# Performance work log

Hardware: AMD Instinct MI355X
Metric: run time of the kernel (lower is better)

The kernel has to match this reference:

```python
import itertools
import jax, jax.numpy as jnp
import numpy as np

B, RES = 256, 16
DIM, KEY_DIM, NUM_HEADS, ATTN_RATIO = 448, 32, 8, 4
SEQ = RES * RES
EXP_KEY_DIM = ATTN_RATIO * KEY_DIM          # 128
TOTAL_KEY = KEY_DIM * NUM_HEADS             # 256
TOTAL_EXP = EXP_KEY_DIM * NUM_HEADS         # 1024
QKV_DIM = TOTAL_EXP + 2 * TOTAL_KEY         # 1536
SCALE = KEY_DIM ** -0.5


def _build_bias_idxs():
    # Replicates the itertools.product loop from build()
    points = list(itertools.product(range(RES), range(RES)))
    offsets = {}
    idxs = []
    for p1 in points:
        for p2 in points:
            off = (abs(p1[0] - p2[0]), abs(p1[1] - p2[1]))
            if off not in offsets:
                offsets[off] = len(offsets)
            idxs.append(offsets[off])
    return np.asarray(idxs, dtype=np.int32).reshape(SEQ, SEQ), len(offsets)


def setup_inputs() -> dict:
    key = jax.random.key(0)
    ks = jax.random.split(key, 6)
    bias_idxs_np, n_off = _build_bias_idxs()
    std = 0.02
    return {
        "hidden_states": jax.random.normal(ks[0], (B, SEQ, DIM), dtype=jnp.float32),
        "qkv_w": jax.random.normal(ks[1], (DIM, QKV_DIM), dtype=jnp.float32) * std,
        "qkv_b": jnp.zeros((QKV_DIM,), dtype=jnp.float32),
        "proj_w": jax.random.normal(ks[2], (TOTAL_EXP, DIM), dtype=jnp.float32) * std,
        "proj_b": jnp.zeros((DIM,), dtype=jnp.float32),
        "attention_biases": jax.random.normal(ks[3], (NUM_HEADS, n_off), dtype=jnp.float32) * std,
        "attention_bias_idxs": jnp.asarray(bias_idxs_np),
    }


def reference(hidden_states, qkv_w, qkv_b, proj_w, proj_b, attention_biases, attention_bias_idxs):
    b, s, _ = hidden_states.shape
    qkv = hidden_states @ qkv_w + qkv_b                       # [B,S,1536]
    qkv = qkv.reshape(b, s, NUM_HEADS, KEY_DIM * 2 + EXP_KEY_DIM)
    q, k, v = jnp.split(qkv, [KEY_DIM, 2 * KEY_DIM], axis=3)  # [B,S,H,dk],[B,S,H,dk],[B,S,H,dv]
    scores = jnp.einsum("bqhd,bkhd->bhqk", q, k) * SCALE      # [B,H,S,S]
    bias = attention_biases[:, attention_bias_idxs]           # [H,S,S] gather
    probs = jax.nn.softmax(scores + bias[None], axis=-1)
    ctx = jnp.einsum("bhqk,bkhd->bqhd", probs, v)             # [B,S,H,dv]
    ctx = ctx.reshape(b, s, TOTAL_EXP)
    return ctx @ proj_w + proj_b
```

## Files before the change

### kernel.cpp

```cpp
#include <hip/hip_runtime.h>
#include <hip/hip_bf16.h>
#include <stdint.h>


typedef __attribute__((ext_vector_type(4))) float f32x4;
typedef __attribute__((ext_vector_type(8))) short short8;
typedef __attribute__((ext_vector_type(4))) unsigned short u16x4;
typedef __attribute__((ext_vector_type(2))) unsigned int u32x2;

#define DEVINL static __device__ __forceinline__

DEVINL unsigned short f2bf(float f) {
  unsigned u = __float_as_uint(f);
  return (unsigned short)((u + 0x7FFFu + ((u >> 16) & 1u)) >> 16);
}
DEVINL float bf2f(short s) {
  return __uint_as_float(((unsigned)(unsigned short)s) << 16);
}
DEVINL unsigned cvt_pk_bf16(float lo, float hi) {
  unsigned r;
  asm("v_cvt_pk_bf16_f32 %0, %1, %2" : "=v"(r) : "v"(lo), "v"(hi));
  return r;
}

DEVINL void gload_lds16(const void* g, void* l) {
  __builtin_amdgcn_global_load_lds((const __attribute__((address_space(1))) void*)g,
                                   (__attribute__((address_space(3))) void*)l,
                                   16, 0, 0);
}

#define SCALE 0.17677669529663687f
#define LOG2E 1.4426950408889634f

#define WS_XB     ((size_t)0)
#define WS_CTX    ((size_t)0)
#define WS_WQT    ((size_t)134217728)
#define WS_WPT    ((size_t)135593984)
#define WS_QW     ((size_t)136642560)
#define WS_KW     ((size_t)170196992)
#define WS_VT     ((size_t)203751424)
#define WS_QKVBP  ((size_t)342163456)

DEVINL int qkv_perm(int np, float* sc) {
  *sc = 1.0f;
  if (np < 512) {
    const int h = np >> 6, c = np & 63;
    if (c < 32) *sc = SCALE * LOG2E;
    return h * 192 + c;
  }
  const int h = (np - 512) >> 7, e = (np - 512) & 127;
  return h * 192 + 64 + e;
}


__global__ void k_convert_x(const float* __restrict__ x, short* __restrict__ xb) {
  const size_t i = (size_t)blockIdx.x * blockDim.x + threadIdx.x;
  const f32x4* src = (const f32x4*)x + i * 2;
  f32x4 a = src[0], b = src[1];
  short8 o;
#pragma unroll
  for (int t = 0; t < 4; ++t) o[t] = (short)f2bf(a[t]);
#pragma unroll
  for (int t = 0; t < 4; ++t) o[4 + t] = (short)f2bf(b[t]);
  ((short8*)xb)[i] = o;
}

__global__ void k_prep_qkvw(const float* __restrict__ w, short* __restrict__ out) {
  const int idx = blockIdx.x * blockDim.x + threadIdx.x;
  if (idx >= 1536 * 448) return;
  const int np = idx / 448, k = idx - np * 448;
  float sc;
  const int n = qkv_perm(np, &sc);
  out[idx] = (short)f2bf(w[(size_t)k * 1536 + n] * sc);
}

__global__ void k_prep_qkvb(const float* __restrict__ bsrc, float* __restrict__ bdst) {
  const int np = blockIdx.x * blockDim.x + threadIdx.x;
  if (np >= 1536) return;
  float sc;
  const int n = qkv_perm(np, &sc);
  bdst[np] = bsrc[n] * sc;
}

__global__ void k_transpose_bf16(const float* __restrict__ in, short* __restrict__ out,
                                 int K, int N, int total) {
  const int idx = blockIdx.x * blockDim.x + threadIdx.x;
  if (idx >= total) return;
  const int n = idx / K, k = idx - n * K;
  const float v = (n < N) ? in[(size_t)k * N + n] : 0.0f;
  out[idx] = (short)f2bf(v);
}


template <int KSTEPS, int LDA, int LDB, bool SWAP>
DEVINL void gemm128_pipe3(const short* __restrict__ A, const short* __restrict__ B,
                          short* Asm , short* Bsm ,
                          int m0, int n0, int tid, f32x4 acc[4][4]) {
  const int lane = tid & 63, wave = tid >> 6;
  const int l15 = lane & 15, g = lane >> 4;
  const int wm = wave >> 1, wn = wave & 1;
  const int r8 = lane >> 3;
  const int scol = (((lane & 7) ^ r8) << 3);
  const int wbase = wave * 32;

  const short* Ab = A + (size_t)(m0 + wbase + r8) * LDA + scol;
  const short* Bb = B + (size_t)(n0 + wbase + r8) * LDB + scol;

  auto stageA = [&](int k) {
    short* dst = Asm + (k % 3) * 8192 + wbase * 64;
    const short* src = Ab + (size_t)k * 64;
#pragma unroll
    for (int c = 0; c < 4; ++c) gload_lds16(src + (size_t)(c * 8) * LDA, dst + c * 512);
    __builtin_amdgcn_sched_barrier(0);
  };
  auto stageB = [&](int k) {
    short* dst = Bsm + (k % 2) * 8192 + wbase * 64;
    const short* src = Bb + (size_t)k * 64;
#pragma unroll
    for (int c = 0; c < 4; ++c) gload_lds16(src + (size_t)(c * 8) * LDB, dst + c * 512);
    __builtin_amdgcn_sched_barrier(0);
  };
  auto compute = [&](int k) {
    const short* Ac = Asm + (k % 3) * 8192;
    const short* Bc = Bsm + (k % 2) * 8192;
#pragma unroll
    for (int s = 0; s < 2; ++s) {
      const int rslot = (((s * 4 + g) ^ (l15 & 7)) << 3);
      short8 a[4], b[4];
#pragma unroll
      for (int i = 0; i < 4; ++i)
        a[i] = *(const short8*)(Ac + (wm * 64 + i * 16 + l15) * 64 + rslot);
#pragma unroll
      for (int j = 0; j < 4; ++j)
        b[j] = *(const short8*)(Bc + (wn * 64 + j * 16 + l15) * 64 + rslot);
#pragma unroll
      for (int i = 0; i < 4; ++i)
#pragma unroll
        for (int j = 0; j < 4; ++j)
          acc[i][j] = SWAP
              ? __builtin_amdgcn_mfma_f32_16x16x32_bf16(b[j], a[i], acc[i][j], 0, 0, 0)
              : __builtin_amdgcn_mfma_f32_16x16x32_bf16(a[i], b[j], acc[i][j], 0, 0, 0);
    }
  };

  stageB(0); stageA(0); stageA(1);
  asm volatile("s_waitcnt vmcnt(4)" ::: "memory");
  __builtin_amdgcn_s_barrier();
  __builtin_amdgcn_sched_barrier(0);

#pragma unroll
  for (int ks = 0; ks < KSTEPS - 2; ++ks) {
    stageB(ks + 1);
    stageA(ks + 2);
    asm volatile("s_waitcnt vmcnt(12)" ::: "memory");
    __builtin_amdgcn_s_barrier();
    __builtin_amdgcn_sched_barrier(0);
    compute(ks);
    __builtin_amdgcn_s_barrier();
  }
  stageB(KSTEPS - 1);
  asm volatile("s_waitcnt vmcnt(8)" ::: "memory");
  __builtin_amdgcn_s_barrier();
  __builtin_amdgcn_sched_barrier(0);
  compute(KSTEPS - 2);
  __builtin_amdgcn_s_barrier();
  asm volatile("s_waitcnt vmcnt(0)" ::: "memory");
  __builtin_amdgcn_s_barrier();
  __builtin_amdgcn_sched_barrier(0);
  compute(KSTEPS - 1);
}


union QkvSmem {
  struct { short a[3 * 8192]; short b[2 * 8192]; } ab;
  short tile[128 * 136];
};

__global__ __launch_bounds__(256) void k_qkv_gemm(
    const short* __restrict__ Xb, const short* __restrict__ Wt,
    const float* __restrict__ qkvbp,
    short* __restrict__ Qw, short* __restrict__ Kw, short* __restrict__ Vt) {
  __shared__ __align__(16) QkvSmem sm;
  const int tid = threadIdx.x;
  const int l = (blockIdx.x & 7) * 768 + (blockIdx.x >> 3);
  const int mt = l / 12, by = l - mt * 12;
  const int m0 = mt * 128, n0 = by * 128;

  const int lane = tid & 63, wave = tid >> 6;
  const int l15 = lane & 15, g = lane >> 4;
  const int wm = wave >> 1, wn = wave & 1;
  const int b0 = m0 >> 8, s0 = m0 & 255;

  f32x4 acc[4][4];
#pragma unroll
  for (int i = 0; i < 4; ++i)
#pragma unroll
    for (int j = 0; j < 4; ++j) acc[i][j] = (f32x4){0.f, 0.f, 0.f, 0.f};

  if (by >= 4) {
    gemm128_pipe3<7, 448, 448, false>(Xb, Wt, sm.ab.a, sm.ab.b, m0, n0, tid, acc);
    __syncthreads();
#pragma unroll
    for (int i = 0; i < 4; ++i) {
#pragma unroll
      for (int j = 0; j < 4; ++j) {
        const float bv = qkvbp[n0 + wn * 64 + j * 16 + l15];
        u16x4 pk;
#pragma unroll
        for (int r = 0; r < 4; ++r) pk[r] = f2bf(acc[i][j][r] + bv);
        *(u16x4*)&sm.tile[(wn * 64 + j * 16 + l15) * 136 + wm * 64 + i * 16 + g * 4] = pk;
      }
    }
    __syncthreads();
    const int bh = b0 * 8 + (by - 4);
#pragma unroll
    for (int p = 0; p < 8; ++p) {
      const int er = p * 16 + (tid >> 4);
      const int sc = (tid & 15) * 8;
      short8 v = *(const short8*)&sm.tile[er * 136 + sc];
      *(short8*)(Vt + (size_t)bh * 33792 + er * 264 + s0 + sc) = v;
    }
  } else {
    gemm128_pipe3<7, 448, 448, true>(Xb, Wt, sm.ab.a, sm.ab.b, m0, n0, tid, acc);
#pragma unroll
    for (int i = 0; i < 4; ++i) {
      const int s = s0 + wm * 64 + i * 16 + l15;
#pragma unroll
      for (int j = 0; j < 4; ++j) {
        const int nbase = n0 + wn * 64 + j * 16 + g * 4;
        const f32x4 bv4 = *(const f32x4*)(qkvbp + nbase);
        u16x4 pk;
#pragma unroll
        for (int r = 0; r < 4; ++r) pk[r] = f2bf(acc[i][j][r] + bv4[r]);
        const int c = nbase & 63;
        const int bh = b0 * 8 + (by << 1) + (nbase >> 6 & 1);
        short* dst = (c < 32) ? (Qw + ((size_t)bh * 256 + s) * 32 + c)
                              : (Kw + ((size_t)bh * 256 + s) * 32 + (c - 32));
        *(u16x4*)dst = pk;
      }
    }
  }
}


__global__ __launch_bounds__(512, 4) void k_attn(
    const short* __restrict__ Qw, const short* __restrict__ Kw,
    const short* __restrict__ Vt, const float* __restrict__ attb, int n_off,
    short* __restrict__ CTX) {
  __shared__ short Ps[4][32 * 264];
  __shared__ float rinv[2][4][32];
  __shared__ float bias_sm[256];

  const int tid = threadIdx.x, lane = tid & 63, wave = tid >> 6;
  const int l15 = lane & 15, g = lane >> 4;
  const int bh = blockIdx.x;
  const int b = bh >> 3, h = bh & 7;

  if (tid < 256) bias_sm[tid] = attb[h * n_off + tid] * LOG2E;
  __syncthreads();

  int offc[4];
#pragma unroll
  for (int r = 0; r < 4; ++r) {
    const int d = g * 4 + r - l15;
    offc[r] = (d < 0) ? -d : d;
  }

  const short* Qb = Qw + (size_t)bh * 8192;
  const short* Kb = Kw + (size_t)bh * 8192;
  const short* Vb = Vt + (size_t)bh * 33792;
  const int e = wave * 16 + l15;

  for (int ph = 0; ph < 2; ++ph) {
    const int Q0 = ph * 128;

    short8 aq[4][2];
#pragma unroll
    for (int u = 0; u < 4; ++u)
#pragma unroll
      for (int i = 0; i < 2; ++i)
        aq[u][i] = *(const short8*)(Qb + (Q0 + u * 32 + i * 16 + l15) * 32 + g * 8);
    short8 bkk[2];
#pragma unroll
    for (int fj = 0; fj < 2; ++fj)
      bkk[fj] = *(const short8*)(Kb + (wave * 32 + fj * 16 + l15) * 32 + g * 8);
    short8 bvv[8];
#pragma unroll
    for (int ks = 0; ks < 8; ++ks)
      bvv[ks] = *(const short8*)(Vb + e * 264 + ks * 32 + g * 8);

#pragma unroll
    for (int fj = 0; fj < 2; ++fj) {
      const int kk0 = wave * 32 + fj * 16;
      const int kr = wave * 2 + fj;
#pragma unroll
      for (int u = 0; u < 4; ++u) {
#pragma unroll
        for (int i = 0; i < 2; ++i) {
          const int qr = ph * 8 + u * 2 + i;
          const int ab = ((qr > kr) ? qr - kr : kr - qr) << 4;
          f32x4 acc;
#pragma unroll
          for (int r = 0; r < 4; ++r) acc[r] = bias_sm[ab + offc[r]];
          acc = __builtin_amdgcn_mfma_f32_16x16x32_bf16(bkk[fj], aq[u][i], acc, 0, 0, 0);
          u32x2 pk;
          pk.x = cvt_pk_bf16(exp2f(acc[0]), exp2f(acc[1]));
          pk.y = cvt_pk_bf16(exp2f(acc[2]), exp2f(acc[3]));
          *(u32x2*)&Ps[u][(i * 16 + l15) * 264 + kk0 + g * 4] = pk;
        }
      }
    }
    __syncthreads();

    {
      const int r = tid >> 4, part = tid & 15;
#pragma unroll
      for (int u = 0; u < 4; ++u) {
        const short* rowp = &Ps[u][r * 264 + part * 16];
        short8 x0 = ((const short8*)rowp)[0];
        short8 x1 = ((const short8*)rowp)[1];
        float sum = 0.f;
#pragma unroll
        for (int t = 0; t < 8; ++t) sum += bf2f(x0[t]) + bf2f(x1[t]);
#pragma unroll
        for (int d = 1; d < 16; d <<= 1) sum += __shfl_xor(sum, d);
        if (part == 0) rinv[ph][u][r] = 1.0f / sum;
      }
    }

    f32x4 cacc[4][2];
#pragma unroll
    for (int u = 0; u < 4; ++u)
#pragma unroll
      for (int qt = 0; qt < 2; ++qt) cacc[u][qt] = (f32x4){0.f, 0.f, 0.f, 0.f};

#pragma unroll
    for (int ks = 0; ks < 8; ++ks) {
#pragma unroll
      for (int u = 0; u < 4; ++u)
#pragma unroll
        for (int qt = 0; qt < 2; ++qt) {
          const short8 ap = *(const short8*)&Ps[u][(qt * 16 + l15) * 264 + ks * 32 + g * 8];
          cacc[u][qt] = __builtin_amdgcn_mfma_f32_16x16x32_bf16(ap, bvv[ks], cacc[u][qt], 0, 0, 0);
        }
    }
    __syncthreads();

#pragma unroll
    for (int u = 0; u < 4; ++u)
#pragma unroll
      for (int qt = 0; qt < 2; ++qt) {
        const int qb = qt * 16 + g * 4;
        const size_t base = ((size_t)b * 256 + Q0 + u * 32 + qb) * 1024 + h * 128 + wave * 16 + l15;
#pragma unroll
        for (int r = 0; r < 4; r += 2) {
          const unsigned pw = cvt_pk_bf16(cacc[u][qt][r] * rinv[ph][u][qb + r],
                                          cacc[u][qt][r + 1] * rinv[ph][u][qb + r + 1]);
          CTX[base + (size_t)r * 1024] = (short)(pw & 0xffffu);
          CTX[base + (size_t)(r + 1) * 1024] = (short)(pw >> 16);
        }
      }
  }
}


__global__ __launch_bounds__(512, 2) void k_proj_gemm(
    const short* __restrict__ CTX, const short* __restrict__ Wpt,
    const float* __restrict__ projb, float* __restrict__ out) {
  __shared__ __align__(16) short Ab[2][2 * 8192];
  __shared__ __align__(16) short Bb[2][2 * 8192];

  const int tid = threadIdx.x, lane = tid & 63, wave = tid >> 6;
  const int l15 = lane & 15, g = lane >> 4;
  const int l = (blockIdx.x & 7) * 64 + (blockIdx.x >> 3);
  const int mt = l >> 1, nt = l & 1;
  const int m0 = mt * 256, n0 = nt * 256;

  const int fmB = (wave & 3) * 2;
  const int fnB = (wave >> 2) * 4;

  const int r8 = lane >> 3;
  const int scol = (((lane & 7) ^ r8) << 3);

  const short* Asrc = CTX + (size_t)m0 * 1024 + scol;
  const short* Bsrc = Wpt + (size_t)n0 * 1024 + scol;

  auto stageA = [&](int kt, int half) {
    short* dst = &Ab[kt & 1][half * 8192];
#pragma unroll
    for (int c = 0; c < 2; ++c) {
      const int row0 = c * 64 + wave * 8;
      gload_lds16(Asrc + (size_t)(half * 128 + row0 + r8) * 1024 + kt * 64,
                  dst + row0 * 64);
    }
    __builtin_amdgcn_sched_barrier(0);
  };
  auto stageB = [&](int kt, int half) {
    short* dst = &Bb[kt & 1][half * 8192];
#pragma unroll
    for (int c = 0; c < 2; ++c) {
      const int row0 = c * 64 + wave * 8;
      gload_lds16(Bsrc + (size_t)(half * 128 + row0 + r8) * 1024 + kt * 64,
                  dst + row0 * 64);
    }
    __builtin_amdgcn_sched_barrier(0);
  };

  f32x4 acc[2][2][2][4];
#pragma unroll
  for (int a = 0; a < 2; ++a)
#pragma unroll
    for (int bq = 0; bq < 2; ++bq)
#pragma unroll
      for (int i = 0; i < 2; ++i)
#pragma unroll
        for (int j = 0; j < 4; ++j) acc[a][bq][i][j] = (f32x4){0.f, 0.f, 0.f, 0.f};

  short8 Ar[2][2][2];
  short8 Br[4][2];

  auto readA = [&](int par, int hm) {
    const short* base = &Ab[par][hm * 8192];
#pragma unroll
    for (int fi = 0; fi < 2; ++fi)
#pragma unroll
      for (int ks = 0; ks < 2; ++ks)
        Ar[hm][fi][ks] = *(const short8*)(base + ((fmB + fi) * 16 + l15) * 64 +
                                          (((ks * 4 + g) ^ (l15 & 7)) << 3));
  };
  auto readB = [&](int par, int hn) {
    const short* base = &Bb[par][hn * 8192];
#pragma unroll
    for (int fi = 0; fi < 4; ++fi)
#pragma unroll
      for (int ks = 0; ks < 2; ++ks)
        Br[fi][ks] = *(const short8*)(base + ((fnB + fi) * 16 + l15) * 64 +
                                      (((ks * 4 + g) ^ (l15 & 7)) << 3));
  };
  auto mfmaQ = [&](int hm, int hn) {
#pragma unroll
    for (int ks = 0; ks < 2; ++ks)
#pragma unroll
      for (int fi = 0; fi < 2; ++fi)
#pragma unroll
        for (int fj = 0; fj < 4; ++fj)
          acc[hm][hn][fi][fj] = __builtin_amdgcn_mfma_f32_16x16x32_bf16(
              Ar[hm][fi][ks], Br[fj][ks], acc[hm][hn][fi][fj], 0, 0, 0);
  };

  stageA(0, 0); stageB(0, 0); stageA(0, 1); stageB(0, 1);

  for (int T = 0; T < 15; ++T) {
    const int par = T & 1;
    stageA(T + 1, 0);
    asm volatile("s_waitcnt vmcnt(6)" ::: "memory");
    __builtin_amdgcn_s_barrier();
    __builtin_amdgcn_sched_barrier(0);
    readA(par, 0); readB(par, 0);
    mfmaQ(0, 0);
    stageB(T + 1, 0);
    asm volatile("s_waitcnt vmcnt(6)" ::: "memory");
    __builtin_amdgcn_s_barrier();
    __builtin_amdgcn_sched_barrier(0);
    readA(par, 1);
    mfmaQ(1, 0);
    stageA(T + 1, 1);
    asm volatile("s_waitcnt vmcnt(6)" ::: "memory");
    __builtin_amdgcn_s_barrier();
    __builtin_amdgcn_sched_barrier(0);
    readB(par, 1);
    mfmaQ(1, 1);
    stageB(T + 1, 1);
    mfmaQ(0, 1);
  }
  {
    asm volatile("s_waitcnt vmcnt(4)" ::: "memory");
    __builtin_amdgcn_s_barrier();
    __builtin_amdgcn_sched_barrier(0);
    readA(1, 0); readB(1, 0);
    mfmaQ(0, 0);
    asm volatile("s_waitcnt vmcnt(2)" ::: "memory");
    __builtin_amdgcn_s_barrier();
    __builtin_amdgcn_sched_barrier(0);
    readA(1, 1);
    mfmaQ(1, 0);
    asm volatile("s_waitcnt vmcnt(0)" ::: "memory");
    __builtin_amdgcn_s_barrier();
    __builtin_amdgcn_sched_barrier(0);
    readB(1, 1);
    mfmaQ(1, 1);
    mfmaQ(0, 1);
  }

#pragma unroll
  for (int hm = 0; hm < 2; ++hm)
#pragma unroll
    for (int hn = 0; hn < 2; ++hn)
#pragma unroll
      for (int fi = 0; fi < 2; ++fi)
#pragma unroll
        for (int fj = 0; fj < 4; ++fj) {
          const int n = n0 + hn * 128 + (fnB + fj) * 16 + l15;
          if (n < 448) {
            const float bv = projb[n];
            const int mb = m0 + hm * 128 + (fmB + fi) * 16 + g * 4;
#pragma unroll
            for (int r = 0; r < 4; ++r)
              out[(size_t)(mb + r) * 448 + n] = acc[hm][hn][fi][fj][r] + bv;
          }
        }
}


extern "C" void kernel_launch(void* const* d_in, const int* in_sizes, int n_in,
                              void* d_out, int out_size, void* d_ws, size_t ws_size,
                              hipStream_t stream) {
  const float* X      = (const float*)d_in[0];
  const float* qkv_w  = (const float*)d_in[1];
  const float* qkv_b  = (const float*)d_in[2];
  const float* proj_w = (const float*)d_in[3];
  const float* proj_b = (const float*)d_in[4];
  const float* att_b  = (const float*)d_in[5];
  const int n_off = in_sizes[5] / 8;

  char* ws = (char*)d_ws;
  short* Xb    = (short*)(ws + WS_XB);
  short* CTX   = (short*)(ws + WS_CTX);
  short* WQT   = (short*)(ws + WS_WQT);
  short* WPT   = (short*)(ws + WS_WPT);
  short* Qw    = (short*)(ws + WS_QW);
  short* Kw    = (short*)(ws + WS_KW);
  short* Vt    = (short*)(ws + WS_VT);
  float* QKVBP = (float*)(ws + WS_QKVBP);

  k_convert_x<<<14336, 256, 0, stream>>>(X, Xb);
  k_prep_qkvw<<<(1536 * 448 + 255) / 256, 256, 0, stream>>>(qkv_w, WQT);
  k_prep_qkvb<<<6, 256, 0, stream>>>(qkv_b, QKVBP);
  k_transpose_bf16<<<(512 * 1024 + 255) / 256, 256, 0, stream>>>(proj_w, WPT, 1024, 448, 512 * 1024);

  k_qkv_gemm<<<6144, 256, 0, stream>>>(Xb, WQT, QKVBP, Qw, Kw, Vt);
  k_attn<<<2048, 512, 0, stream>>>(Qw, Kw, Vt, att_b, n_off, CTX);
  k_proj_gemm<<<512, 512, 0, stream>>>(CTX, WPT, proj_b, (float*)d_out);
}
```

Baseline: 334.9 us.

## Switch QKV GEMM to 256x256 tiles using shared proj GEMM pipeline

Moves the QKV projection GEMM from 128x128 tiles on 256-thread blocks to 256x256 tiles on 512-thread blocks. It reuses the double-buffered, quarter-interleaved pipeline from the proj GEMM, now pulled into a shared Gemm256 template. The larger tile is meant to cut global/L2 traffic per FLOP and reduce block count. The V output now goes straight from registers to the transposed layout instead of through an LDS transpose, which may give less coalesced stores. Tiles now span whole heads and batches, and the Q/K vs V split shifts from column tile 4 to 2.

```diff
diff --git a/kernel.cpp b/kernel.cpp
--- a/kernel.cpp
+++ b/kernel.cpp
@@ -92,153 +92,192 @@
 }
 
 
-template <int KSTEPS, int LDA, int LDB, bool SWAP>
-DEVINL void gemm128_pipe3(const short* __restrict__ A, const short* __restrict__ B,
-                          short* Asm , short* Bsm ,
-                          int m0, int n0, int tid, f32x4 acc[4][4]) {
-  const int lane = tid & 63, wave = tid >> 6;
-  const int l15 = lane & 15, g = lane >> 4;
-  const int wm = wave >> 1, wn = wave & 1;
-  const int r8 = lane >> 3;
-  const int scol = (((lane & 7) ^ r8) << 3);
-  const int wbase = wave * 32;
-
-  const short* Ab = A + (size_t)(m0 + wbase + r8) * LDA + scol;
-  const short* Bb = B + (size_t)(n0 + wbase + r8) * LDB + scol;
-
-  auto stageA = [&](int k) {
-    short* dst = Asm + (k % 3) * 8192 + wbase * 64;
-    const short* src = Ab + (size_t)k * 64;
-#pragma unroll
-    for (int c = 0; c < 4; ++c) gload_lds16(src + (size_t)(c * 8) * LDA, dst + c * 512);
-    __builtin_amdgcn_sched_barrier(0);
-  };
-  auto stageB = [&](int k) {
-    short* dst = Bsm + (k % 2) * 8192 + wbase * 64;
-    const short* src = Bb + (size_t)k * 64;
-#pragma unroll
-    for (int c = 0; c < 4; ++c) gload_lds16(src + (size_t)(c * 8) * LDB, dst + c * 512);
-    __builtin_amdgcn_sched_barrier(0);
-  };
-  auto compute = [&](int k) {
-    const short* Ac = Asm + (k % 3) * 8192;
-    const short* Bc = Bsm + (k % 2) * 8192;
-#pragma unroll
-    for (int s = 0; s < 2; ++s) {
-      const int rslot = (((s * 4 + g) ^ (l15 & 7)) << 3);
-      short8 a[4], b[4];
-#pragma unroll
-      for (int i = 0; i < 4; ++i)
-        a[i] = *(const short8*)(Ac + (wm * 64 + i * 16 + l15) * 64 + rslot);
-#pragma unroll
-      for (int j = 0; j < 4; ++j)
-        b[j] = *(const short8*)(Bc + (wn * 64 + j * 16 + l15) * 64 + rslot);
-#pragma unroll
-      for (int i = 0; i < 4; ++i)
-#pragma unroll
-        for (int j = 0; j < 4; ++j)
-          acc[i][j] = SWAP
-              ? __builtin_amdgcn_mfma_f32_16x16x32_bf16(b[j], a[i], acc[i][j], 0, 0, 0)
-              : __builtin_amdgcn_mfma_f32_16x16x32_bf16(a[i], b[j], acc[i][j], 0, 0, 0);
+template <int KSTEPS, int LD, bool SWAP>
+struct Gemm256 {
+  DEVINL static void run(const short* __restrict__ A, const short* __restrict__ B,
+                         short (*Ab)[2 * 8192], short (*Bb)[2 * 8192],
+                         int m0, int n0, int tid, f32x4 acc[2][2][2][4]) {
+    const int lane = tid & 63, wave = tid >> 6;
+    const int l15 = lane & 15, g = lane >> 4;
+    const int fmB = (wave & 3) * 2;
+    const int fnB = (wave >> 2) * 4;
+    const int r8 = lane >> 3;
+    const int scol = (((lane & 7) ^ r8) << 3);
+
+    const short* Asrc = A + (size_t)m0 * LD + scol;
+    const short* Bsrc = B + (size_t)n0 * LD + scol;
+
+    auto stageA = [&](int kt, int half) {
+      short* dst = &Ab[kt & 1][half * 8192];
+#pragma unroll
+      for (int c = 0; c < 2; ++c) {
+        const int row0 = c * 64 + wave * 8;
+        gload_lds16(Asrc + (size_t)(half * 128 + row0 + r8) * LD + kt * 64,
+                    dst + row0 * 64);
+      }
+      __builtin_amdgcn_sched_barrier(0);
+    };
+    auto stageB = [&](int kt, int half) {
+      short* dst = &Bb[kt & 1][half * 8192];
+#pragma unroll
+      for (int c = 0; c < 2; ++c) {
+        const int row0 = c * 64 + wave * 8;
+        gload_lds16(Bsrc + (size_t)(half * 128 + row0 + r8) * LD + kt * 64,
+                    dst + row0 * 64);
+      }
+      __builtin_amdgcn_sched_barrier(0);
+    };
+
+    short8 Ar[2][2][2];
+    short8 Br[4][2];
+
+    auto readA = [&](int par, int hm) {
+#pragma unroll
+      for (int fi = 0; fi < 2; ++fi)
+#pragma unroll
+        for (int ks = 0; ks < 2; ++ks)
+          Ar[hm][fi][ks] = *(const short8*)(&Ab[par][hm * 8192] +
+              ((fmB + fi) * 16 + l15) * 64 + (((ks * 4 + g) ^ (l15 & 7)) << 3));
+    };
+    auto readB = [&](int par, int hn) {
+#pragma unroll
+      for (int fj = 0; fj < 4; ++fj)
+#pragma unroll
+        for (int ks = 0; ks < 2; ++ks)
+          Br[fj][ks] = *(const short8*)(&Bb[par][hn * 8192] +
+              ((fnB + fj) * 16 + l15) * 64 + (((ks * 4 + g) ^ (l15 & 7)) << 3));
+    };
+    auto mfmaQ = [&](int hm, int hn) {
+#pragma unroll
+      for (int ks = 0; ks < 2; ++ks)
+#pragma unroll
+        for (int fi = 0; fi < 2; ++fi)
+#pragma unroll
+          for (int fj = 0; fj < 4; ++fj)
+            acc[hm][hn][fi][fj] = SWAP
+                ? __builtin_amdgcn_mfma_f32_16x16x32_bf16(Br[fj][ks], Ar[hm][fi][ks],
+                                                          acc[hm][hn][fi][fj], 0, 0, 0)
+                : __builtin_amdgcn_mfma_f32_16x16x32_bf16(Ar[hm][fi][ks], Br[fj][ks],
+                                                          acc[hm][hn][fi][fj], 0, 0, 0);
+    };
+
+    stageA(0, 0); stageB(0, 0); stageA(0, 1); stageB(0, 1);
+
+    for (int T = 0; T < KSTEPS - 1; ++T) {
+      const int par = T & 1;
+      stageA(T + 1, 0);
+      asm volatile("s_waitcnt vmcnt(6)" ::: "memory");
+      __builtin_amdgcn_s_barrier();
+      __builtin_amdgcn_sched_barrier(0);
+      readA(par, 0); readB(par, 0);
+      mfmaQ(0, 0);
+      stageB(T + 1, 0);
+      asm volatile("s_waitcnt vmcnt(6)" ::: "memory");
+      __builtin_amdgcn_s_barrier();
+      __builtin_amdgcn_sched_barrier(0);
+      readA(par, 1);
+      mfmaQ(1, 0);
+      stageA(T + 1, 1);
+      asm volatile("s_waitcnt vmcnt(6)" ::: "memory");
+      __builtin_amdgcn_s_barrier();
+      __builtin_amdgcn_sched_barrier(0);
+      readB(par, 1);
+      mfmaQ(1, 1);
+      stageB(T + 1, 1);
+      mfmaQ(0, 1);
     }
-  };
-
-  stageB(0); stageA(0); stageA(1);
-  asm volatile("s_waitcnt vmcnt(4)" ::: "memory");
-  __builtin_amdgcn_s_barrier();
-  __builtin_amdgcn_sched_barrier(0);
-
-#pragma unroll
-  for (int ks = 0; ks < KSTEPS - 2; ++ks) {
-    stageB(ks + 1);
-    stageA(ks + 2);
-    asm volatile("s_waitcnt vmcnt(12)" ::: "memory");
-    __builtin_amdgcn_s_barrier();
-    __builtin_amdgcn_sched_barrier(0);
-    compute(ks);
-    __builtin_amdgcn_s_barrier();
+    {
+      const int fpar = (KSTEPS - 1) & 1;
+      asm volatile("s_waitcnt vmcnt(4)" ::: "memory");
+      __builtin_amdgcn_s_barrier();
+      __builtin_amdgcn_sched_barrier(0);
+      readA(fpar, 0); readB(fpar, 0);
+      mfmaQ(0, 0);
+      asm volatile("s_waitcnt vmcnt(2)" ::: "memory");
+      __builtin_amdgcn_s_barrier();
+      __builtin_amdgcn_sched_barrier(0);
+      readA(fpar, 1);
+      mfmaQ(1, 0);
+      asm volatile("s_waitcnt vmcnt(0)" ::: "memory");
+      __builtin_amdgcn_s_barrier();
+      __builtin_amdgcn_sched_barrier(0);
+      readB(fpar, 1);
+      mfmaQ(1, 1);
+      mfmaQ(0, 1);
+    }
   }
-  stageB(KSTEPS - 1);
-  asm volatile("s_waitcnt vmcnt(8)" ::: "memory");
-  __builtin_amdgcn_s_barrier();
-  __builtin_amdgcn_sched_barrier(0);
-  compute(KSTEPS - 2);
-  __builtin_amdgcn_s_barrier();
-  asm volatile("s_waitcnt vmcnt(0)" ::: "memory");
-  __builtin_amdgcn_s_barrier();
-  __builtin_amdgcn_sched_barrier(0);
-  compute(KSTEPS - 1);
-}
-
-
-union QkvSmem {
-  struct { short a[3 * 8192]; short b[2 * 8192]; } ab;
-  short tile[128 * 136];
 };
 
-__global__ __launch_bounds__(256) void k_qkv_gemm(
+
+__global__ __launch_bounds__(512, 2) void k_qkv_gemm(
     const short* __restrict__ Xb, const short* __restrict__ Wt,
     const float* __restrict__ qkvbp,
     short* __restrict__ Qw, short* __restrict__ Kw, short* __restrict__ Vt) {
-  __shared__ __align__(16) QkvSmem sm;
-  const int tid = threadIdx.x;
-  const int l = (blockIdx.x & 7) * 768 + (blockIdx.x >> 3);
-  const int mt = l / 12, by = l - mt * 12;
-  const int m0 = mt * 128, n0 = by * 128;
-
-  const int lane = tid & 63, wave = tid >> 6;
+  __shared__ __align__(16) short Ab[2][2 * 8192];
+  __shared__ __align__(16) short Bb[2][2 * 8192];
+
+  const int tid = threadIdx.x, lane = tid & 63, wave = tid >> 6;
   const int l15 = lane & 15, g = lane >> 4;
-  const int wm = wave >> 1, wn = wave & 1;
-  const int b0 = m0 >> 8, s0 = m0 & 255;
-
-  f32x4 acc[4][4];
-#pragma unroll
-  for (int i = 0; i < 4; ++i)
-#pragma unroll
-    for (int j = 0; j < 4; ++j) acc[i][j] = (f32x4){0.f, 0.f, 0.f, 0.f};
-
-  if (by >= 4) {
-    gemm128_pipe3<7, 448, 448, false>(Xb, Wt, sm.ab.a, sm.ab.b, m0, n0, tid, acc);
-    __syncthreads();
-#pragma unroll
-    for (int i = 0; i < 4; ++i) {
-#pragma unroll
-      for (int j = 0; j < 4; ++j) {
-        const float bv = qkvbp[n0 + wn * 64 + j * 16 + l15];
-        u16x4 pk;
-#pragma unroll
-        for (int r = 0; r < 4; ++r) pk[r] = f2bf(acc[i][j][r] + bv);
-        *(u16x4*)&sm.tile[(wn * 64 + j * 16 + l15) * 136 + wm * 64 + i * 16 + g * 4] = pk;
-      }
-    }
-    __syncthreads();
-    const int bh = b0 * 8 + (by - 4);
-#pragma unroll
-    for (int p = 0; p < 8; ++p) {
-      const int er = p * 16 + (tid >> 4);
-      const int sc = (tid & 15) * 8;
-      short8 v = *(const short8*)&sm.tile[er * 136 + sc];
-      *(short8*)(Vt + (size_t)bh * 33792 + er * 264 + s0 + sc) = v;
-    }
+  const int l = (blockIdx.x & 7) * 192 + (blockIdx.x >> 3);
+  const int mt = l / 6, nt = l - mt * 6;
+  const int m0 = mt * 256, n0 = nt * 256;
+
+  const int fmB = (wave & 3) * 2;
+  const int fnB = (wave >> 2) * 4;
+
+  f32x4 acc[2][2][2][4];
+#pragma unroll
+  for (int a = 0; a < 2; ++a)
+#pragma unroll
+    for (int bq = 0; bq < 2; ++bq)
+#pragma unroll
+      for (int i = 0; i < 2; ++i)
+#pragma unroll
+        for (int j = 0; j < 4; ++j) acc[a][bq][i][j] = (f32x4){0.f, 0.f, 0.f, 0.f};
+
+  if (nt < 2) {
+    Gemm256<7, 448, true>::run(Xb, Wt, Ab, Bb, m0, n0, tid, acc);
+#pragma unroll
+    for (int hm = 0; hm < 2; ++hm)
+#pragma unroll
+      for (int hn = 0; hn < 2; ++hn)
+#pragma unroll
+        for (int fi = 0; fi < 2; ++fi)
+#pragma unroll
+          for (int fj = 0; fj < 4; ++fj) {
+            const int s = hm * 128 + (fmB + fi) * 16 + l15;
+            const int nb = n0 + hn * 128 + (fnB + fj) * 16 + g * 4;
+            const f32x4 bv4 = *(const f32x4*)(qkvbp + nb);
+            u16x4 pk;
+#pragma unroll
+            for (int r = 0; r < 4; ++r) pk[r] = f2bf(acc[hm][hn][fi][fj][r] + bv4[r]);
+            const int h = nb >> 6, c = nb & 63;
+            const int bh = mt * 8 + h;
+            short* dst = (c < 32) ? (Qw + ((size_t)bh * 256 + s) * 32 + c)
+                                  : (Kw + ((size_t)bh * 256 + s) * 32 + (c - 32));
+            *(u16x4*)dst = pk;
+          }
   } else {
-    gemm128_pipe3<7, 448, 448, true>(Xb, Wt, sm.ab.a, sm.ab.b, m0, n0, tid, acc);
-#pragma unroll
-    for (int i = 0; i < 4; ++i) {
-      const int s = s0 + wm * 64 + i * 16 + l15;
-#pragma unroll
-      for (int j = 0; j < 4; ++j) {
-        const int nbase = n0 + wn * 64 + j * 16 + g * 4;
-        const f32x4 bv4 = *(const f32x4*)(qkvbp + nbase);
-        u16x4 pk;
-#pragma unroll
-        for (int r = 0; r < 4; ++r) pk[r] = f2bf(acc[i][j][r] + bv4[r]);
-        const int c = nbase & 63;
-        const int bh = b0 * 8 + (by << 1) + (nbase >> 6 & 1);
-        short* dst = (c < 32) ? (Qw + ((size_t)bh * 256 + s) * 32 + c)
-                              : (Kw + ((size_t)bh * 256 + s) * 32 + (c - 32));
-        *(u16x4*)dst = pk;
-      }
-    }
+    Gemm256<7, 448, false>::run(Xb, Wt, Ab, Bb, m0, n0, tid, acc);
+#pragma unroll
+    for (int hm = 0; hm < 2; ++hm)
+#pragma unroll
+      for (int hn = 0; hn < 2; ++hn)
+#pragma unroll
+        for (int fi = 0; fi < 2; ++fi)
+#pragma unroll
+          for (int fj = 0; fj < 4; ++fj) {
+            const int np = n0 + hn * 128 + (fnB + fj) * 16 + l15;
+            const float bv = qkvbp[np];
+            const int idx = np - 512;
+            const int h = idx >> 7, e = idx & 127;
+            const int bh = mt * 8 + h;
+            const int s = hm * 128 + (fmB + fi) * 16 + g * 4;
+            u16x4 pk;
+#pragma unroll
+            for (int r = 0; r < 4; ++r) pk[r] = f2bf(acc[hm][hn][fi][fj][r] + bv);
+            *(u16x4*)(Vt + (size_t)bh * 33792 + e * 264 + s) = pk;
+          }
   }
 }
 
@@ -379,33 +418,6 @@
   const int fmB = (wave & 3) * 2;
   const int fnB = (wave >> 2) * 4;
 
-  const int r8 = lane >> 3;
-  const int scol = (((lane & 7) ^ r8) << 3);
-
-  const short* Asrc = CTX + (size_t)m0 * 1024 + scol;
-  const short* Bsrc = Wpt + (size_t)n0 * 1024 + scol;
-
-  auto stageA = [&](int kt, int half) {
-    short* dst = &Ab[kt & 1][half * 8192];
-#pragma unroll
-    for (int c = 0; c < 2; ++c) {
-      const int row0 = c * 64 + wave * 8;
-      gload_lds16(Asrc + (size_t)(half * 128 + row0 + r8) * 1024 + kt * 64,
-                  dst + row0 * 64);
-    }
-    __builtin_amdgcn_sched_barrier(0);
-  };
-  auto stageB = [&](int kt, int half) {
-    short* dst = &Bb[kt & 1][half * 8192];
-#pragma unroll
-    for (int c = 0; c < 2; ++c) {
-      const int row0 = c * 64 + wave * 8;
-      gload_lds16(Bsrc + (size_t)(half * 128 + row0 + r8) * 1024 + kt * 64,
-                  dst + row0 * 64);
-    }
-    __builtin_amdgcn_sched_barrier(0);
-  };
-
   f32x4 acc[2][2][2][4];
 #pragma unroll
   for (int a = 0; a < 2; ++a)
@@ -416,81 +428,7 @@
 #pragma unroll
         for (int j = 0; j < 4; ++j) acc[a][bq][i][j] = (f32x4){0.f, 0.f, 0.f, 0.f};
 
-  short8 Ar[2][2][2];
-  short8 Br[4][2];
-
-  auto readA = [&](int par, int hm) {
-    const short* base = &Ab[par][hm * 8192];
-#pragma unroll
-    for (int fi = 0; fi < 2; ++fi)
-#pragma unroll
-      for (int ks = 0; ks < 2; ++ks)
-        Ar[hm][fi][ks] = *(const short8*)(base + ((fmB + fi) * 16 + l15) * 64 +
-                                          (((ks * 4 + g) ^ (l15 & 7)) << 3));
-  };
-  auto readB = [&](int par, int hn) {
-    const short* base = &Bb[par][hn * 8192];
-#pragma unroll
-    for (int fi = 0; fi < 4; ++fi)
-#pragma unroll
-      for (int ks = 0; ks < 2; ++ks)
-        Br[fi][ks] = *(const short8*)(base + ((fnB + fi) * 16 + l15) * 64 +
-                                      (((ks * 4 + g) ^ (l15 & 7)) << 3));
-  };
-  auto mfmaQ = [&](int hm, int hn) {
-#pragma unroll
-    for (int ks = 0; ks < 2; ++ks)
-#pragma unroll
-      for (int fi = 0; fi < 2; ++fi)
-#pragma unroll
-        for (int fj = 0; fj < 4; ++fj)
-          acc[hm][hn][fi][fj] = __builtin_amdgcn_mfma_f32_16x16x32_bf16(
-              Ar[hm][fi][ks], Br[fj][ks], acc[hm][hn][fi][fj], 0, 0, 0);
-  };
-
-  stageA(0, 0); stageB(0, 0); stageA(0, 1); stageB(0, 1);
-
-  for (int T = 0; T < 15; ++T) {
-    const int par = T & 1;
-    stageA(T + 1, 0);
-    asm volatile("s_waitcnt vmcnt(6)" ::: "memory");
-    __builtin_amdgcn_s_barrier();
-    __builtin_amdgcn_sched_barrier(0);
-    readA(par, 0); readB(par, 0);
-    mfmaQ(0, 0);
-    stageB(T + 1, 0);
-    asm volatile("s_waitcnt vmcnt(6)" ::: "memory");
-    __builtin_amdgcn_s_barrier();
-    __builtin_amdgcn_sched_barrier(0);
-    readA(par, 1);
-    mfmaQ(1, 0);
-    stageA(T + 1, 1);
-    asm volatile("s_waitcnt vmcnt(6)" ::: "memory");
-    __builtin_amdgcn_s_barrier();
-    __builtin_amdgcn_sched_barrier(0);
-    readB(par, 1);
-    mfmaQ(1, 1);
-    stageB(T + 1, 1);
-    mfmaQ(0, 1);
-  }
-  {
-    asm volatile("s_waitcnt vmcnt(4)" ::: "memory");
-    __builtin_amdgcn_s_barrier();
-    __builtin_amdgcn_sched_barrier(0);
-    readA(1, 0); readB(1, 0);
-    mfmaQ(0, 0);
-    asm volatile("s_waitcnt vmcnt(2)" ::: "memory");
-    __builtin_amdgcn_s_barrier();
-    __builtin_amdgcn_sched_barrier(0);
-    readA(1, 1);
-    mfmaQ(1, 0);
-    asm volatile("s_waitcnt vmcnt(0)" ::: "memory");
-    __builtin_amdgcn_s_barrier();
-    __builtin_amdgcn_sched_barrier(0);
-    readB(1, 1);
-    mfmaQ(1, 1);
-    mfmaQ(0, 1);
-  }
+  Gemm256<16, 1024, false>::run(CTX, Wpt, Ab, Bb, m0, n0, tid, acc);
 
 #pragma unroll
   for (int hm = 0; hm < 2; ++hm)
@@ -538,7 +476,7 @@
   k_prep_qkvb<<<6, 256, 0, stream>>>(qkv_b, QKVBP);
   k_transpose_bf16<<<(512 * 1024 + 255) / 256, 256, 0, stream>>>(proj_w, WPT, 1024, 448, 512 * 1024);
 
-  k_qkv_gemm<<<6144, 256, 0, stream>>>(Xb, WQT, QKVBP, Qw, Kw, Vt);
+  k_qkv_gemm<<<1536, 512, 0, stream>>>(Xb, WQT, QKVBP, Qw, Kw, Vt);
   k_attn<<<2048, 512, 0, stream>>>(Qw, Kw, Vt, att_b, n_off, CTX);
   k_proj_gemm<<<512, 512, 0, stream>>>(CTX, WPT, proj_b, (float*)d_out);
 }
```

Result: slower. 347.0 us (+3.6%).
